# Performance work log

Measured on AMD Instinct MI355X. Metric: run time of the kernel, lower is better.

Reference implementation:

```python
import math
import jax, jax.numpy as jnp
import numpy as np

NUM_CLASSES = 80
CONF_THR = 0.05
IOU_THR = 0.5
MAX_PER_CLASS = 100
MAX_DET = 100
PRE_NMS_K = 200  # per-class candidates kept before greedy NMS (>= max_per_class)
BOX_VAR = np.array([0.1, 0.1, 0.2, 0.2], np.float32)
IMG_H, IMG_W = 640, 640
BATCH = 8


def _anchor_dims():
    ratios = [0.5, 1.0, 2.0]
    scales = [2.0 ** x for x in (0.0, 1.0 / 3.0, 2.0 / 3.0)]
    dims_all = []
    for area in [32.0 ** 2, 64.0 ** 2, 128.0 ** 2, 256.0 ** 2, 512.0 ** 2]:
        dims = []
        for r in ratios:  # ratio-major, scale-minor (matches AnchorBox._compute_dims)
            h = math.sqrt(area / r)
            w = area / h
            for s in scales:
                dims.append([s * w, s * h])
        dims_all.append(np.array(dims, np.float32))  # [9, 2]
    return dims_all


def get_anchors(H, W):
    """Anchors in [cx, cy, w, h], shape [total_anchors, 4] (static, numpy)."""
    strides = [8, 16, 32, 64, 128]
    out = []
    for stride, dims in zip(strides, _anchor_dims()):
        fh, fw = math.ceil(H / stride), math.ceil(W / stride)
        rx = (np.arange(fw, dtype=np.float32) + 0.5) * stride
        ry = (np.arange(fh, dtype=np.float32) + 0.5) * stride
        cx, cy = np.meshgrid(rx, ry)  # each [fh, fw], 'xy' indexing like tf.meshgrid
        centers = np.broadcast_to(np.stack([cx, cy], -1)[:, :, None, :], (fh, fw, 9, 2))
        d = np.broadcast_to(dims[None, None], (fh, fw, 9, 2))
        out.append(np.concatenate([centers, d], -1).reshape(-1, 4))
    return jnp.asarray(np.concatenate(out, 0))


def decode_boxes(anchors, box_pred):
    """Apply variance scaling + anchor offsets, return corner boxes."""
    b = box_pred * jnp.asarray(BOX_VAR)
    xy = b[..., :2] * anchors[..., 2:] + anchors[..., :2]
    wh = jnp.exp(b[..., 2:]) * anchors[..., 2:]
    return jnp.concatenate([xy - wh * 0.5, xy + wh * 0.5], axis=-1)


def pairwise_iou(b):
    lt = jnp.maximum(b[:, None, :2], b[None, :, :2])
    rb = jnp.minimum(b[:, None, 2:], b[None, :, 2:])
    wh = jnp.maximum(rb - lt, 0.0)
    inter = wh[..., 0] * wh[..., 1]
    area = (b[:, 2] - b[:, 0]) * (b[:, 3] - b[:, 1])
    return inter / (area[:, None] + area[None, :] - inter + 1e-8)


def nms_one_class(boxes, scores):
    """Greedy NMS over top PRE_NMS_K candidates for one class."""
    sc, idx = jax.lax.top_k(scores, PRE_NMS_K)
    bb = boxes[idx]  # [K, 4]
    valid = sc > CONF_THR
    iou = jax.lax.stop_gradient(pairwise_iou(bb))  # [K, K]
    ar = jnp.arange(PRE_NMS_K)

    def body(i, keep):
        supp = keep[i] & (iou[i] > IOU_THR) & (ar > i)
        return keep & ~supp

    keep = jax.lax.fori_loop(0, PRE_NMS_K, body, valid)
    sc = jnp.where(keep, sc, 0.0)
    sc2, j = jax.lax.top_k(sc, MAX_PER_CLASS)
    bb2 = jnp.where((sc2 > 0.0)[:, None], bb[j], 0.0)
    return bb2, sc2


def detect_one_image(boxes, cls_scores):
    """boxes [A,4] shared across classes, cls_scores [A,C]."""
    cb, cs = jax.vmap(nms_one_class, in_axes=(None, 1))(boxes, cls_scores)  # [C,100,4],[C,100]
    cls_id = jnp.broadcast_to(
        jnp.arange(NUM_CLASSES, dtype=jnp.float32)[:, None], cs.shape
    )
    flat_s = cs.reshape(-1)
    flat_b = cb.reshape(-1, 4)
    flat_c = cls_id.reshape(-1)
    s, i = jax.lax.top_k(flat_s, MAX_DET)
    b = jnp.where((s > 0.0)[:, None], flat_b[i], 0.0)
    c = jnp.where(s > 0.0, flat_c[i], 0.0)
    n = jnp.sum(s > 0.0).astype(jnp.int32)
    return b, s, c, n


def setup_inputs() -> dict:
    key = jax.random.key(0)
    k1, _ = jax.random.split(key)
    images = jnp.zeros((BATCH, IMG_H, IMG_W, 3), jnp.float32)  # only shape is used
    num_anchors = 76725  # 640x640 image -> (6400+1600+400+100+25)*9
    predictions = jax.random.normal(k1, (BATCH, num_anchors, 4 + NUM_CLASSES), jnp.float32)
    return {"images": images, "predictions": predictions}


def reference(images, predictions):
    H, W = images.shape[1], images.shape[2]
    anchors = get_anchors(H, W)  # [A, 4]
    box_pred = predictions[:, :, :4]
    cls_pred = jax.nn.sigmoid(predictions[:, :, 4:])  # [B, A, C]
    boxes = decode_boxes(anchors[None], box_pred)  # [B, A, 4]
    nmsed_boxes, nmsed_scores, nmsed_classes, valid = jax.vmap(detect_one_image)(
        boxes, cls_pred
    )
    return nmsed_boxes, nmsed_scores, nmsed_classes, valid
```

## Files before the change

### kernel.cpp

```cpp
#include <hip/hip_runtime.h>
#include <stdint.h>

typedef unsigned long long u64;
typedef unsigned int u32;
typedef unsigned char u8;

#define NB 8
#define NA 76725
#define NC 80
#define NCH 84
#define PRE_K 200
#define MAXPC 100
#define MAXDET 100
#define F4_PER_IMG (NA * 21u)

#define T0 0.93f
#define XCUT 2.58f
#define BLKX 256
#define SPAN (BLKX * 256u)
#define NSTEP 24
#define LCAP 24
#define CAP2 512
#define CAPF 2048


__device__ __forceinline__ float sigmoid_ref(float x) {
    return 1.0f / (1.0f + expf(-x));
}

__device__ void decode_box(float4 d, int a, float4* box, float* areaOut) {
    int lvl, off, fw, stride;
    if (a < 57600)      { lvl = 0; off = 0;     fw = 80; stride = 8;   }
    else if (a < 72000) { lvl = 1; off = 57600; fw = 40; stride = 16;  }
    else if (a < 75600) { lvl = 2; off = 72000; fw = 20; stride = 32;  }
    else if (a < 76500) { lvl = 3; off = 75600; fw = 10; stride = 64;  }
    else                { lvl = 4; off = 76500; fw = 5;  stride = 128; }
    int idx  = a - off;
    int k    = idx % 9;
    int cell = idx / 9;
    int row = cell / fw, col = cell - row * fw;
    float cx = __fmul_rn((float)col + 0.5f, (float)stride);
    float cy = __fmul_rn((float)row + 0.5f, (float)stride);
    int ri = k / 3, si = k - ri * 3;
    double r    = (ri == 0) ? 0.5 : ((ri == 1) ? 1.0 : 2.0);
    double side = (double)(32 << lvl);
    double area = side * side;
    double h = sqrt(area / r);
    double w = area / h;
    double s = exp2((double)si / 3.0);
    float aw = (float)(s * w);
    float ah = (float)(s * h);
    float b0 = __fmul_rn(d.x, 0.1f);
    float b1 = __fmul_rn(d.y, 0.1f);
    float b2 = __fmul_rn(d.z, 0.2f);
    float b3 = __fmul_rn(d.w, 0.2f);
    float ux = __fadd_rn(__fmul_rn(b0, aw), cx);
    float uy = __fadd_rn(__fmul_rn(b1, ah), cy);
    float wx = __fmul_rn(expf(b2), aw);
    float wy = __fmul_rn(expf(b3), ah);
    float hx = __fmul_rn(wx, 0.5f);
    float hy = __fmul_rn(wy, 0.5f);
    float x1 = __fsub_rn(ux, hx), y1 = __fsub_rn(uy, hy);
    float x2 = __fadd_rn(ux, hx), y2 = __fadd_rn(uy, hy);
    *box = make_float4(x1, y1, x2, y2);
    *areaOut = __fmul_rn(__fsub_rn(x2, x1), __fsub_rn(y2, y1));
}


__device__ __forceinline__ void scan4(float4 v, u32 idx,
                                      u32* lhist, u64 (*llist)[LCAP]) {
    u32 a  = idx / 21u;
    u32 c4 = idx - a * 21u;
    if (c4 == 0u) return;
    float m = fmaxf(fmaxf(v.x, v.y), fmaxf(v.z, v.w));
    if (m <= XCUT) return;
    u32 cb = c4 * 4u - 4u;
    float vv[4] = {v.x, v.y, v.z, v.w};
#pragma unroll
    for (int q = 0; q < 4; ++q) {
        if (vv[q] > XCUT) {
            float sig = sigmoid_ref(vv[q]);
            if (sig > T0) {
                u32 c = cb + (u32)q;
                u64 key = ((u64)__float_as_uint(sig) << 32) | (u64)(~a);
                u32 p = atomicAdd(&lhist[c], 1u);
                if (p < LCAP) llist[c][p] = key;
            }
        }
    }
}

__global__ __launch_bounds__(256, 4) void k_scan(const float4* __restrict__ p4,
                                                 u64* __restrict__ seg,
                                                 u32* __restrict__ cntT) {
    __shared__ u32 lhist[NC];
    __shared__ u64 llist[NC][LCAP];
    u32 b = blockIdx.y, x = blockIdx.x;
    for (u32 c = threadIdx.x; c < NC; c += 256u) lhist[c] = 0u;
    __syncthreads();

    const float4* base = p4 + (u64)b * F4_PER_IMG;
    u32 i0 = x * 256u + threadIdx.x;
#pragma unroll 1
    for (int s = 0; s < NSTEP; s += 4) {
        u32 ia = i0 + (u32)s * SPAN;
        float4 v0 = base[ia];
        float4 v1 = base[ia + SPAN];
        float4 v2 = base[ia + 2u * SPAN];
        float4 v3 = base[ia + 3u * SPAN];
        scan4(v0, ia,            lhist, llist);
        scan4(v1, ia + SPAN,     lhist, llist);
        scan4(v2, ia + 2u*SPAN,  lhist, llist);
        scan4(v3, ia + 3u*SPAN,  lhist, llist);
    }
    {
        u32 it = i0 + (u32)NSTEP * SPAN;
        if (it < F4_PER_IMG) scan4(base[it], it, lhist, llist);
    }
    __syncthreads();

    if (threadIdx.x < NC) {
        u32 c = threadIdx.x;
        u32 n = lhist[c];
        u32 m = n < LCAP ? n : (u32)LCAP;
        u64* o = seg + ((u64)(b * NC + c) * BLKX + x) * LCAP;
        for (u32 j = 0; j < m; ++j) o[j] = llist[c][j];
        cntT[(b * NC + c) * BLKX + x] = n;
    }
}


__global__ __launch_bounds__(256) void k_nms(const float* __restrict__ pred,
                                             const u64* __restrict__ seg,
                                             const u32* __restrict__ cntT,
                                             float* __restrict__ sc2,
                                             float* __restrict__ bb2) {
    int bc = blockIdx.x;
    int b = bc / NC, c = bc % NC;
    __shared__ u64 keys[CAP2];
    __shared__ u64 sorted[PRE_K];
    __shared__ u32 wsum[4];
    __shared__ u32 oflow[4];
    __shared__ float4 box[PRE_K];
    __shared__ float area[PRE_K];
    __shared__ u32 validw[8];
    __shared__ u32 keepw[8];
    __shared__ u32 chg;
    __shared__ u64 red[256];

    u32 tid = threadIdx.x, lane = tid & 63u, wv = tid >> 6;

    u32 n_raw = cntT[(u64)bc * BLKX + tid];
    u32 m_c = n_raw < LCAP ? n_raw : (u32)LCAP;
    u32 v = m_c;
#pragma unroll
    for (u32 d = 1; d < 64u; d <<= 1) {
        u32 t = __shfl_up(v, d, 64);
        if (lane >= d) v += t;
    }
    u64 ob = __ballot(n_raw > (u32)LCAP);
    if (lane == 63u) wsum[wv] = v;
    if (lane == 0u)  oflow[wv] = (ob != 0ull) ? 1u : 0u;
    __syncthreads();
    u32 off = 0;
    for (u32 w = 0; w < wv; ++w) off += wsum[w];
    u32 inc = v + off;
    u32 total = wsum[0] + wsum[1] + wsum[2] + wsum[3];
    bool over = (oflow[0] | oflow[1] | oflow[2] | oflow[3]) != 0u;
    bool repaired = over || (total < (u32)PRE_K) || (total > (u32)CAP2);

    if (!repaired) {
        u32 dst = inc - m_c;
        const u64* src = seg + ((u64)bc * BLKX + tid) * LCAP;
        for (u32 j = 0; j < m_c; ++j) keys[dst + j] = src[j];
        __syncthreads();
        u64 ka = (tid < total) ? keys[tid] : 0ull;
        u64 kb = (tid + 256u < total) ? keys[tid + 256u] : 0ull;
        u32 ra = 0, rb = 0;
        for (u32 j = 0; j < total; ++j) {
            u64 kj = keys[j];
            ra += (kj > ka) ? 1u : 0u;
            rb += (kj > kb) ? 1u : 0u;
        }
        if (tid < total && ra < (u32)PRE_K) sorted[ra] = ka;
        if (tid + 256u < total && rb < (u32)PRE_K) sorted[rb] = kb;
        __syncthreads();
    } else {
        u64 cur = ~0ull;
        for (int k = 0; k < PRE_K; ++k) {
            u64 loc = 0;
            for (int a = tid; a < NA; a += 256) {
                float xx = pred[((long)b * NA + a) * NCH + 4 + c];
                float sg = sigmoid_ref(xx);
                u64 key  = ((u64)__float_as_uint(sg) << 32) | (u64)(~(u32)a);
                if (key < cur && key > loc) loc = key;
            }
            red[tid] = loc;
            __syncthreads();
            for (int s = 128; s > 0; s >>= 1) {
                if (tid < (u32)s) {
                    if (red[tid + s] > red[tid]) red[tid] = red[tid + s];
                }
                __syncthreads();
            }
            cur = red[0];
            if (tid == 0) sorted[k] = cur;
            __syncthreads();
        }
    }

    bool val = false;
    float4 mybox = make_float4(0.f, 0.f, 0.f, 0.f);
    float myarea = 0.f;
    if (tid < (u32)PRE_K) {
        u64 key = sorted[tid];
        float sig = __uint_as_float((u32)(key >> 32));
        int a = (int)(~(u32)key);
        if (sig > 0.05f) {
            float4 dd = *(const float4*)(pred + ((long)b * NA + a) * NCH);
            decode_box(dd, a, &mybox, &myarea);
            val = true;
        }
        box[tid] = mybox; area[tid] = myarea;
    }
    u64 vbal = __ballot(val);
    if (lane == 0u) {
        validw[2u * wv]      = (u32)vbal;
        validw[2u * wv + 1u] = (u32)(vbal >> 32);
        keepw[2u * wv]       = (u32)vbal;
        keepw[2u * wv + 1u]  = (u32)(vbal >> 32);
    }
    __syncthreads();

    u32 rsup[7];
#pragma unroll
    for (int w = 0; w < 7; ++w) {
        u32 m = 0;
        if (val && (u32)(w * 32) < tid) {
            for (int ii = 0; ii < 32; ++ii) {
                int i = w * 32 + ii;
                if ((u32)i < tid) {
                    float4 bi = box[i];
                    float ai = area[i];
                    float ltx = fmaxf(bi.x, mybox.x), lty = fmaxf(bi.y, mybox.y);
                    float rbx = fminf(bi.z, mybox.z), rby = fminf(bi.w, mybox.w);
                    float wx = fmaxf(__fsub_rn(rbx, ltx), 0.f);
                    float wy = fmaxf(__fsub_rn(rby, lty), 0.f);
                    float inter = __fmul_rn(wx, wy);
                    float den = __fadd_rn(__fsub_rn(__fadd_rn(ai, myarea), inter), 1e-8f);
                    float iou = __fdiv_rn(inter, den);
                    if (iou > 0.5f) m |= 1u << ii;
                }
            }
        }
        rsup[w] = m;
    }
    __syncthreads();

    for (int t = 0; t < PRE_K; ++t) {
        if (tid == 0) chg = 0u;
        __syncthreads();
        u32 k0 = keepw[0], k1 = keepw[1], k2 = keepw[2], k3 = keepw[3];
        u32 k4 = keepw[4], k5 = keepw[5], k6 = keepw[6];
        bool nb = false;
        if (val) {
            u32 sup = (k0 & rsup[0]) | (k1 & rsup[1]) | (k2 & rsup[2]) |
                      (k3 & rsup[3]) | (k4 & rsup[4]) | (k5 & rsup[5]) |
                      (k6 & rsup[6]);
            nb = (sup == 0u);
        }
        u64 bal = __ballot(nb);
        u64 oldk = ((u64)keepw[2u * wv + 1u] << 32) | (u64)keepw[2u * wv];
        if (lane == 0u) {
            keepw[2u * wv]      = (u32)bal;
            keepw[2u * wv + 1u] = (u32)(bal >> 32);
            if (bal != oldk) chg = 1u;
        }
        __syncthreads();
        u32 cflag = chg;
        __syncthreads();
        if (cflag == 0u) break;
    }

    int kept = 0;
#pragma unroll
    for (int w = 0; w < 7; ++w) kept += __popc(keepw[w]);
    if (kept > MAXPC) kept = MAXPC;

    if (tid >= (u32)kept && tid < (u32)MAXPC) {
        int pos = tid;
        sc2[bc * MAXPC + pos] = 0.f;
        float* o = bb2 + ((long)bc * MAXPC + pos) * 4;
        o[0] = 0.f; o[1] = 0.f; o[2] = 0.f; o[3] = 0.f;
    }
    if (tid < (u32)PRE_K) {
        int r = tid;
        if ((keepw[r >> 5] >> (r & 31)) & 1u) {
            int pos = 0;
            for (int w = 0; w < (r >> 5); ++w) pos += __popc(keepw[w]);
            pos += __popc(keepw[r >> 5] & ((1u << (r & 31)) - 1u));
            if (pos < MAXPC) {
                u64 key = sorted[r];
                float sig = __uint_as_float((u32)(key >> 32));
                sc2[bc * MAXPC + pos] = sig;
                float* o = bb2 + ((long)bc * MAXPC + pos) * 4;
                o[0] = mybox.x; o[1] = mybox.y; o[2] = mybox.z; o[3] = mybox.w;
            }
        }
    }
}


__global__ __launch_bounds__(1024) void k_final(const float* __restrict__ sc2,
                                                const float* __restrict__ bb2,
                                                float* __restrict__ out) {
    int b = blockIdx.x;
    __shared__ u32 hist[256];
    __shared__ u32 sfx[256];
    __shared__ u64 keys[CAPF];
    __shared__ u64 top[128];
    __shared__ u32 cnt_s;
    __shared__ int t_s;
    __shared__ u64 red[1024];

    for (int i = threadIdx.x; i < 256; i += blockDim.x) hist[i] = 0u;
    if (threadIdx.x < 128) top[threadIdx.x] = 0ull;
    if (threadIdx.x == 0) { cnt_s = 0u; t_s = 0; }
    __syncthreads();

    const float* s_b = sc2 + b * (NC * MAXPC);
    for (int f = threadIdx.x; f < NC * MAXPC; f += blockDim.x) {
        float s = s_b[f];
        if (s > 0.f) {
            int bin = (int)(s * 256.f); if (bin > 255) bin = 255;
            atomicAdd(&hist[bin], 1u);
        }
    }
    __syncthreads();

    if (threadIdx.x < 256) sfx[threadIdx.x] = hist[threadIdx.x];
    __syncthreads();
    for (u32 d = 1; d < 256u; d <<= 1) {
        u32 v = 0;
        if (threadIdx.x < 256u && threadIdx.x + d < 256u) v = sfx[threadIdx.x + d];
        __syncthreads();
        if (threadIdx.x < 256u) sfx[threadIdx.x] += v;
        __syncthreads();
    }
    if (threadIdx.x < 256) {
        bool ge = sfx[threadIdx.x] >= (u32)MAXDET;
        bool nlt = (threadIdx.x == 255) || (sfx[threadIdx.x + 1] < (u32)MAXDET);
        if (ge && nlt) t_s = (int)threadIdx.x;
    }
    __syncthreads();
    int t = t_s;

    for (int f = threadIdx.x; f < NC * MAXPC; f += blockDim.x) {
        float s = s_b[f];
        if (s > 0.f) {
            int bin = (int)(s * 256.f); if (bin > 255) bin = 255;
            if (bin >= t) {
                u32 pos = atomicAdd(&cnt_s, 1u);
                if (pos < CAPF)
                    keys[pos] = ((u64)__float_as_uint(s) << 32) | (u64)(~(u32)f);
            }
        }
    }
    __syncthreads();
    u32 g = cnt_s;

    if (g <= (u32)CAPF) {
        u64 ka = (threadIdx.x < g) ? keys[threadIdx.x] : 0ull;
        u64 kb = (threadIdx.x + 1024u < g) ? keys[threadIdx.x + 1024u] : 0ull;
        u32 ra = 0, rb = 0;
        for (u32 j = 0; j < g; ++j) {
            u64 kj = keys[j];
            ra += (kj > ka) ? 1u : 0u;
            rb += (kj > kb) ? 1u : 0u;
        }
        if (threadIdx.x < g && ra < (u32)MAXDET) top[ra] = ka;
        if (threadIdx.x + 1024u < g && rb < (u32)MAXDET) top[rb] = kb;
        __syncthreads();
    } else {
        u64 cur = ~0ull;
        for (int k = 0; k < MAXDET; ++k) {
            u64 loc = 0;
            for (int f = threadIdx.x; f < NC * MAXPC; f += blockDim.x) {
                float s = s_b[f];
                if (s > 0.f) {
                    u64 key = ((u64)__float_as_uint(s) << 32) | (u64)(~(u32)f);
                    if (key < cur && key > loc) loc = key;
                }
            }
            red[threadIdx.x] = loc;
            __syncthreads();
            for (int st = 512; st > 0; st >>= 1) {
                if (threadIdx.x < (u32)st) {
                    if (red[threadIdx.x + st] > red[threadIdx.x])
                        red[threadIdx.x] = red[threadIdx.x + st];
                }
                __syncthreads();
            }
            cur = red[0];
            if (threadIdx.x == 0) top[k] = cur;
            __syncthreads();
        }
        if (threadIdx.x == 0) {
            u32 nv = 0;
            for (int r = 0; r < MAXDET; ++r) if (top[r] != 0ull) ++nv;
            cnt_s = nv;
        }
        __syncthreads();
        g = cnt_s;
    }

    if (threadIdx.x < MAXDET) {
        int r = threadIdx.x;
        u64 key = top[r];
        u32 hi = (u32)(key >> 32);
        float s = 0.f, cf = 0.f;
        float bx0 = 0.f, bx1 = 0.f, bx2 = 0.f, bx3 = 0.f;
        if (hi != 0u) {
            s = __uint_as_float(hi);
            int f = (int)(~(u32)key);
            int c = f / MAXPC, jj = f - c * MAXPC;
            const float* bsrc = bb2 + ((long)(b * NC + c) * MAXPC + jj) * 4;
            bx0 = bsrc[0]; bx1 = bsrc[1]; bx2 = bsrc[2]; bx3 = bsrc[3];
            cf = (float)c;
        }
        float* ob = out + ((long)b * MAXDET + r) * 4;
        ob[0] = bx0; ob[1] = bx1; ob[2] = bx2; ob[3] = bx3;
        out[NB * MAXDET * 4 + b * MAXDET + r] = s;
        out[NB * MAXDET * 4 + NB * MAXDET + b * MAXDET + r] = cf;
    }
    if (threadIdx.x == 0) {
        u32 nv = g < (u32)MAXDET ? g : (u32)MAXDET;
        out[NB * MAXDET * 4 + 2 * NB * MAXDET + b] = (float)nv;
    }
}


extern "C" void kernel_launch(void* const* d_in, const int* in_sizes, int n_in,
                              void* d_out, int out_size, void* d_ws, size_t ws_size,
                              hipStream_t stream) {
    const float* pred = (const float*)d_in[1];
    if (n_in >= 2 && in_sizes[0] == NB * NA * NCH) pred = (const float*)d_in[0];

    char* ws = (char*)d_ws;
    const long BCN = (long)NB * NC;
    u64* seg   = (u64*)ws;
    char* p    = ws + BCN * BLKX * LCAP * 8;
    u32* cntT  = (u32*)p;            p += BCN * BLKX * 4;
    float* sc2 = (float*)p;          p += BCN * MAXPC * 4;
    float* bb2 = (float*)p;

    k_scan <<<dim3(BLKX, NB), 256, 0, stream>>>((const float4*)pred, seg, cntT);
    k_nms  <<<dim3(NB * NC),  256, 0, stream>>>(pred, seg, cntT, sc2, bb2);
    k_final<<<dim3(NB),      1024, 0, stream>>>(sc2, bb2, (float*)d_out);
}
```

Measured before the change: 111.0 us.

## Run greedy NMS fixed-point iteration in a single wavefront without block barriers

The iterative keep-mask fixed-point loop, which needed several __syncthreads per iteration across four wavefronts, now runs entirely inside one 64-lane wavefront. Each lane holds suppression bitmasks for up to four candidates in registers, loaded from a new shared rsupA array, and uses ballots to rebuild the keep mask. Box areas are recomputed inline instead of being stored in shared memory. This removes per-iteration block barriers and shared-memory traffic, at the cost of extra shared memory for the mask table and three idle wavefronts during the loop.

```diff
diff --git a/kernel.cpp b/kernel.cpp
--- a/kernel.cpp
+++ b/kernel.cpp
@@ -142,10 +142,9 @@
     __shared__ u32 wsum[4];
     __shared__ u32 oflow[4];
     __shared__ float4 box[PRE_K];
-    __shared__ float area[PRE_K];
+    __shared__ u32 rsupA[PRE_K][8];
     __shared__ u32 validw[8];
     __shared__ u32 keepw[8];
-    __shared__ u32 chg;
     __shared__ u64 red[256];
 
     u32 tid = threadIdx.x, lane = tid & 63u, wv = tid >> 6;
@@ -221,14 +220,12 @@
             decode_box(dd, a, &mybox, &myarea);
             val = true;
         }
-        box[tid] = mybox; area[tid] = myarea;
+        box[tid] = mybox;
     }
     u64 vbal = __ballot(val);
     if (lane == 0u) {
         validw[2u * wv]      = (u32)vbal;
         validw[2u * wv + 1u] = (u32)(vbal >> 32);
-        keepw[2u * wv]       = (u32)vbal;
-        keepw[2u * wv + 1u]  = (u32)(vbal >> 32);
     }
     __syncthreads();
 
@@ -241,7 +238,7 @@
                 int i = w * 32 + ii;
                 if ((u32)i < tid) {
                     float4 bi = box[i];
-                    float ai = area[i];
+                    float ai = __fmul_rn(__fsub_rn(bi.z, bi.x), __fsub_rn(bi.w, bi.y));
                     float ltx = fmaxf(bi.x, mybox.x), lty = fmaxf(bi.y, mybox.y);
                     float rbx = fminf(bi.z, mybox.z), rby = fminf(bi.w, mybox.w);
                     float wx = fmaxf(__fsub_rn(rbx, ltx), 0.f);
@@ -255,32 +252,63 @@
         }
         rsup[w] = m;
     }
-    __syncthreads();
-
-    for (int t = 0; t < PRE_K; ++t) {
-        if (tid == 0) chg = 0u;
-        __syncthreads();
-        u32 k0 = keepw[0], k1 = keepw[1], k2 = keepw[2], k3 = keepw[3];
-        u32 k4 = keepw[4], k5 = keepw[5], k6 = keepw[6];
-        bool nb = false;
-        if (val) {
-            u32 sup = (k0 & rsup[0]) | (k1 & rsup[1]) | (k2 & rsup[2]) |
-                      (k3 & rsup[3]) | (k4 & rsup[4]) | (k5 & rsup[5]) |
-                      (k6 & rsup[6]);
-            nb = (sup == 0u);
-        }
-        u64 bal = __ballot(nb);
-        u64 oldk = ((u64)keepw[2u * wv + 1u] << 32) | (u64)keepw[2u * wv];
-        if (lane == 0u) {
-            keepw[2u * wv]      = (u32)bal;
-            keepw[2u * wv + 1u] = (u32)(bal >> 32);
-            if (bal != oldk) chg = 1u;
-        }
-        __syncthreads();
-        u32 cflag = chg;
-        __syncthreads();
-        if (cflag == 0u) break;
-    }
+    if (tid < (u32)PRE_K) {
+#pragma unroll
+        for (int w = 0; w < 7; ++w) rsupA[tid][w] = rsup[w];
+        rsupA[tid][7] = 0u;
+    }
+    __syncthreads();
+
+    if (tid < 64u) {
+        u32 l = tid;
+        uint4 sA0 = *(const uint4*)&rsupA[l][0];
+        uint4 sA1 = *(const uint4*)&rsupA[l][4];
+        uint4 sB0 = *(const uint4*)&rsupA[l + 64u][0];
+        uint4 sB1 = *(const uint4*)&rsupA[l + 64u][4];
+        uint4 sC0 = *(const uint4*)&rsupA[l + 128u][0];
+        uint4 sC1 = *(const uint4*)&rsupA[l + 128u][4];
+        uint4 sD0 = make_uint4(0u, 0u, 0u, 0u);
+        uint4 sD1 = make_uint4(0u, 0u, 0u, 0u);
+        if (l < 8u) {
+            sD0 = *(const uint4*)&rsupA[l + 192u][0];
+            sD1 = *(const uint4*)&rsupA[l + 192u][4];
+        }
+        u32 v0 = validw[0], v1 = validw[1], v2 = validw[2], v3 = validw[3];
+        u32 v4 = validw[4], v5 = validw[5], v6 = validw[6];
+        u32 vb0 = (u32)(((((u64)v1 << 32) | v0) >> l) & 1ull);
+        u32 vb1 = (u32)(((((u64)v3 << 32) | v2) >> l) & 1ull);
+        u32 vb2 = (u32)(((((u64)v5 << 32) | v4) >> l) & 1ull);
+        u32 vb3 = (l < 8u) ? ((v6 >> l) & 1u) : 0u;
+        u32 k0 = v0, k1 = v1, k2 = v2, k3 = v3, k4 = v4, k5 = v5, k6 = v6;
+        for (int t = 0; t < PRE_K; ++t) {
+            u32 s0 = (k0 & sA0.x) | (k1 & sA0.y) | (k2 & sA0.z) | (k3 & sA0.w)
+                   | (k4 & sA1.x) | (k5 & sA1.y) | (k6 & sA1.z);
+            u32 s1 = (k0 & sB0.x) | (k1 & sB0.y) | (k2 & sB0.z) | (k3 & sB0.w)
+                   | (k4 & sB1.x) | (k5 & sB1.y) | (k6 & sB1.z);
+            u32 s2 = (k0 & sC0.x) | (k1 & sC0.y) | (k2 & sC0.z) | (k3 & sC0.w)
+                   | (k4 & sC1.x) | (k5 & sC1.y) | (k6 & sC1.z);
+            u32 s3 = (k0 & sD0.x) | (k1 & sD0.y) | (k2 & sD0.z) | (k3 & sD0.w)
+                   | (k4 & sD1.x) | (k5 & sD1.y) | (k6 & sD1.z);
+            bool n0 = vb0 && (s0 == 0u);
+            bool n1 = vb1 && (s1 == 0u);
+            bool n2 = vb2 && (s2 == 0u);
+            bool n3 = (vb3 != 0u) && (s3 == 0u);
+            u64 B0 = __ballot(n0), B1 = __ballot(n1), B2 = __ballot(n2), B3 = __ballot(n3);
+            u32 nk0 = (u32)B0, nk1 = (u32)(B0 >> 32);
+            u32 nk2 = (u32)B1, nk3 = (u32)(B1 >> 32);
+            u32 nk4 = (u32)B2, nk5 = (u32)(B2 >> 32);
+            u32 nk6 = (u32)B3;
+            bool same = (nk0 == k0) && (nk1 == k1) && (nk2 == k2) && (nk3 == k3)
+                     && (nk4 == k4) && (nk5 == k5) && (nk6 == k6);
+            k0 = nk0; k1 = nk1; k2 = nk2; k3 = nk3; k4 = nk4; k5 = nk5; k6 = nk6;
+            if (same) break;
+        }
+        if (l == 0u) {
+            keepw[0] = k0; keepw[1] = k1; keepw[2] = k2; keepw[3] = k3;
+            keepw[4] = k4; keepw[5] = k5; keepw[6] = k6;
+        }
+    }
+    __syncthreads();
 
     int kept = 0;
 #pragma unroll
```

After: 110.8 us. Within noise of the previous version (-0.2%).
